# Optimization experiments

Measured on AMD Instinct MI355X. Metric: run time of the kernel, lower is better.

Reference implementation:

```python
import jax, jax.numpy as jnp
import numpy as np

B, C, O, H, W = 4, 64, 64, 96, 320


def _conv(x, w, b):
    # NCHW conv, stride 1, SAME padding (matches pad=kernel//2 in the torch code)
    out = jax.lax.conv_general_dilated(x, w, (1, 1), 'SAME',
                                       dimension_numbers=('NCHW', 'OIHW', 'NCHW'))
    return out + b[None, :, None, None]


def setup_inputs() -> dict:
    key = jax.random.key(0)
    ks = jax.random.split(key, 18)
    s = 0.05  # small init so learned offsets stay in a realistic few-pixel range
    d = {}
    d['x'] = jax.random.normal(ks[0], (B, C, H, W), jnp.float32)
    d['scale_box2d'] = jax.random.uniform(ks[1], (B, 5), jnp.float32, 0.0, 100.0)
    d['glob_w1'] = jax.random.normal(ks[2], (64, 2), jnp.float32) * s
    d['glob_b1'] = jnp.zeros((64,), jnp.float32)
    d['glob_w2'] = jax.random.normal(ks[3], (32, 64), jnp.float32) * s
    d['glob_b2'] = jnp.zeros((32,), jnp.float32)
    d['loc_w1'] = jax.random.normal(ks[4], (32, C, 3, 3), jnp.float32) * s
    d['loc_b1'] = jnp.zeros((32,), jnp.float32)
    d['loc_w2'] = jax.random.normal(ks[5], (32, 32, 1, 1), jnp.float32) * s
    d['loc_b2'] = jnp.zeros((32,), jnp.float32)
    d['fuse_w1'] = jax.random.normal(ks[6], (32, 64, 3, 3), jnp.float32) * s
    d['fuse_b1'] = jnp.zeros((32,), jnp.float32)
    d['fuse_w2'] = jax.random.normal(ks[7], (18, 32, 1, 1), jnp.float32) * s
    d['fuse_b2'] = jnp.zeros((18,), jnp.float32)
    d['mask_w'] = jnp.full((9, C, 3, 3), 0.5, jnp.float32)  # matches init_mask in torch code
    d['mask_b'] = jnp.zeros((9,), jnp.float32)
    d['conv_w'] = jax.random.normal(ks[8], (O, C, 3, 3), jnp.float32) * s
    d['conv_b'] = jax.random.normal(ks[9], (O,), jnp.float32) * s
    return d


def _deform_conv2d(x, offset, mask, weight, bias):
    # torchvision.ops.deform_conv2d, 3x3 kernel, stride 1, pad 1, dilation 1,
    # one offset group. offset channels are (dy, dx) interleaved per kernel tap.
    b, c, h, w = x.shape
    K = 9
    off = offset.reshape(b, K, 2, h, w)
    dy, dx = off[:, :, 0], off[:, :, 1]            # [B,K,H,W]
    ki = jnp.arange(3, dtype=jnp.float32) - 1.0     # kernel tap offsets with pad=1
    ky = jnp.repeat(ki, 3)                          # [9] row-major taps
    kx = jnp.tile(ki, 3)
    ys = jnp.arange(h, dtype=jnp.float32)[None, None, :, None] + ky[None, :, None, None] + dy
    xs = jnp.arange(w, dtype=jnp.float32)[None, None, None, :] + kx[None, :, None, None] + dx

    y0 = jnp.floor(ys).astype(jnp.int32)
    x0 = jnp.floor(xs).astype(jnp.int32)
    wy = (ys - y0.astype(jnp.float32))[:, None]     # [B,1,K,H,W]
    wx = (xs - x0.astype(jnp.float32))[:, None]

    xf = x.reshape(b, c, h * w)

    def gather(yi, xi):
        valid = ((yi >= 0) & (yi < h) & (xi >= 0) & (xi < w))
        yc = jnp.clip(yi, 0, h - 1)
        xc = jnp.clip(xi, 0, w - 1)
        idx = (yc * w + xc).reshape(b, 1, K * h * w)
        g = jnp.take_along_axis(xf, idx, axis=2).reshape(b, c, K, h, w)
        return g * valid.astype(x.dtype)[:, None]

    val = (gather(y0, x0) * (1 - wy) * (1 - wx)
           + gather(y0, x0 + 1) * (1 - wy) * wx
           + gather(y0 + 1, x0) * wy * (1 - wx)
           + gather(y0 + 1, x0 + 1) * wy * wx)   # [B,C,K,H,W]

    val = val * mask[:, None]                      # modulation mask [B,1,K,H,W]
    out = jnp.einsum('bckhw,ock->bohw', val, weight.reshape(weight.shape[0], c, K))
    return out + bias[None, :, None, None]


def reference(x, scale_box2d, glob_w1, glob_b1, glob_w2, glob_b2,
              loc_w1, loc_b1, loc_w2, loc_b2,
              fuse_w1, fuse_b1, fuse_w2, fuse_b2,
              mask_w, mask_b, conv_w, conv_b):
    b, c, h, w = x.shape
    bsize = jnp.stack([scale_box2d[:, 4] - scale_box2d[:, 2],
                       scale_box2d[:, 3] - scale_box2d[:, 1]], axis=-1)  # [B,2]
    g = jax.nn.relu(bsize @ glob_w1.T + glob_b1) @ glob_w2.T + glob_b2   # [B,32]
    g_offset = jnp.broadcast_to(g[:, :, None, None], (b, 32, h, w))
    l = _conv(jax.nn.relu(_conv(x, loc_w1, loc_b1)), loc_w2, loc_b2)     # [B,32,H,W]
    f = jax.nn.relu(_conv(jnp.concatenate([g_offset, l], axis=1), fuse_w1, fuse_b1))
    offset = _conv(f, fuse_w2, fuse_b2)                                  # [B,18,H,W]
    mask = jax.nn.sigmoid(_conv(x, mask_w, mask_b))                      # [B,9,H,W]
    return _deform_conv2d(x, offset, mask, conv_w, conv_b)
```

## Files before the change

kernel.cpp:

```cpp
#include <hip/hip_runtime.h>
#include <hip/hip_bf16.h>
#include <math.h>

#define BB 4
#define CC 64
#define OO 64
#define HH 96
#define WW 320
#define HWP (HH*WW)
#define NPIX (BB*HWP)

typedef __attribute__((ext_vector_type(8))) short bf16x8;
typedef __attribute__((ext_vector_type(8))) unsigned short u16x8;
typedef __attribute__((ext_vector_type(4))) float f32x4;

__device__ inline unsigned short f2bf(float f) {
    unsigned int u = __float_as_uint(f);
    u = (u + 0x7FFFu + ((u >> 16) & 1u)) >> 16;
    return (unsigned short)u;
}
__device__ inline float bf2f(unsigned short s) {
    return __uint_as_float(((unsigned int)s) << 16);
}
__device__ inline unsigned int pack2bf(float lo, float hi) {
    return (__float_as_uint(lo) >> 16) | (__float_as_uint(hi) & 0xffff0000u);
}

#define PREP_N (36864 + 27648 + 1024 + 9216 + 1024)
__global__ void k_prep(const float* __restrict__ cw,
                       const float* __restrict__ lw1, const float* __restrict__ mw,
                       const float* __restrict__ lw2,
                       const float* __restrict__ fw1, const float* __restrict__ fw2,
                       unsigned short* __restrict__ cwT,
                       unsigned short* __restrict__ Wlm,
                       unsigned short* __restrict__ lw2T,
                       unsigned short* __restrict__ Wf,
                       unsigned short* __restrict__ fw2A) {
    int e = blockIdx.x * 256 + threadIdx.x;
    if (e < 36864) {
        int k = e >> 12, r = e & 4095, o = r >> 6, ci = r & 63;
        cwT[e] = f2bf(cw[o * 576 + ci * 9 + k]);
        return;
    }
    e -= 36864;
    if (e < 27648) {
        int k = e / 3072, r = e % 3072, row = r >> 6, ci = r & 63;
        float v = 0.f;
        if (row < 32) v = lw1[row * 576 + ci * 9 + k];
        else if (row < 41) v = mw[(row - 32) * 576 + ci * 9 + k];
        Wlm[e] = f2bf(v);
        return;
    }
    e -= 27648;
    if (e < 1024) { lw2T[e] = f2bf(lw2[e]); return; }
    e -= 1024;
    if (e < 9216) {
        int k = e >> 10, r = e & 1023, o = r >> 5, cl = r & 31;
        Wf[e] = f2bf(fw1[o * 576 + (32 + cl) * 9 + k]);
        return;
    }
    e -= 9216;
    if (e < 1024) {
        int m = e >> 5, ci = e & 31;
        fw2A[e] = f2bf(m < 18 ? fw2[m * 32 + ci] : 0.f);
    }
}

__global__ void k_glob(const float* __restrict__ sb,
                       const float* __restrict__ gw1, const float* __restrict__ gb1,
                       const float* __restrict__ gw2, const float* __restrict__ gb2,
                       const float* __restrict__ fw1,
                       float* __restrict__ gsum) {
    __shared__ float g_s[BB * 32];
    int tid = threadIdx.x;
    if (tid < 128) {
        int b = tid >> 5, i = tid & 31;
        float b0 = sb[b * 5 + 4] - sb[b * 5 + 2];
        float b1 = sb[b * 5 + 3] - sb[b * 5 + 1];
        float acc = gb2[i];
        for (int j = 0; j < 64; ++j) {
            float h1 = b0 * gw1[j * 2 + 0] + b1 * gw1[j * 2 + 1] + gb1[j];
            h1 = fmaxf(h1, 0.f);
            acc += gw2[i * 64 + j] * h1;
        }
        g_s[b * 32 + i] = acc;
    }
    __syncthreads();
    for (int e = tid; e < BB * 32 * 9; e += blockDim.x) {
        int b = e / 288, r = e % 288, o = r / 9, k = r % 9;
        float s = 0.f;
        for (int ci = 0; ci < 32; ++ci)
            s += g_s[b * 32 + ci] * fw1[o * 576 + ci * 9 + k];
        gsum[e] = s;
    }
}

__global__ __launch_bounds__(256) void k_xT(const float* __restrict__ x,
                                            unsigned short* __restrict__ xT) {
    __shared__ unsigned short Ls[64 * 66];
    int tid = threadIdx.x;
    int p0 = blockIdx.x * 64;
    int b = p0 / HWP;
    int rem0 = p0 % HWP;
    int px = tid & 63;
    int g4 = tid >> 6;
    const float* xb = x + (size_t)b * CC * HWP + rem0;
#pragma unroll
    for (int it = 0; it < 16; ++it) {
        int ci = it * 4 + g4;
        Ls[px * 66 + ci] = f2bf(xb[(size_t)ci * HWP + px]);
    }
    __syncthreads();
#pragma unroll
    for (int it = 0; it < 16; ++it) {
        int p = it * 4 + g4;
        xT[(size_t)(p0 + p) * 64 + px] = Ls[p * 66 + px];
    }
}

__global__ __launch_bounds__(256) void k_locmask(
        const unsigned short* __restrict__ xT,
        const unsigned short* __restrict__ Wlm,
        const unsigned short* __restrict__ lw2T,
        const float* __restrict__ lb1, const float* __restrict__ lb2,
        const float* __restrict__ mb,
        unsigned short* __restrict__ lT, unsigned short* __restrict__ mbuf) {
    __shared__ unsigned short Vs[128 * 72];
    __shared__ unsigned short Ws[48 * 72];
    __shared__ unsigned short VsL[128 * 40];
    __shared__ unsigned short W2[32 * 40];

    int tid = threadIdx.x;
    int p0 = blockIdx.x * 128;
    int rem0 = p0 % HWP;

    int lane = tid & 63, wv = tid >> 6;
    int lr = lane & 15, lq = lane >> 4;
    int n0 = wv * 32;

    int spx = tid >> 1;
    int shf = tid & 1;
    int sy = (rem0 + spx) / WW;
    int sx = (rem0 + spx) % WW;

    f32x4 acc[3][2];
#pragma unroll
    for (int mt = 0; mt < 3; ++mt)
#pragma unroll
        for (int t = 0; t < 2; ++t) acc[mt][t] = (f32x4){0.f, 0.f, 0.f, 0.f};

    for (int k = 0; k < 9; ++k) {
        int dy = k / 3 - 1, dx = k % 3 - 1;
        __syncthreads();
#pragma unroll
        for (int c = tid; c < 384; c += 256) {
            int row = c >> 3, g = c & 7;
            *(float4*)&Ws[row * 72 + g * 8] =
                *(const float4*)&Wlm[((size_t)k * 48 + row) * 64 + g * 8];
        }
        {
            int yy = sy + dy, xw = sx + dx;
            bool valid = (yy >= 0) && (yy < HH) && (xw >= 0) && (xw < WW);
            unsigned short* dst = &Vs[spx * 72 + shf * 32];
            if (valid) {
                const unsigned short* src =
                    xT + ((size_t)(p0 + spx) + (dy * WW + dx)) * 64 + shf * 32;
#pragma unroll
                for (int j = 0; j < 4; ++j)
                    *(float4*)(dst + j * 8) = *(const float4*)(src + j * 8);
            } else {
                float4 z = {0.f, 0.f, 0.f, 0.f};
#pragma unroll
                for (int j = 0; j < 4; ++j) *(float4*)(dst + j * 8) = z;
            }
        }
        __syncthreads();
#pragma unroll
        for (int h = 0; h < 2; ++h) {
            bf16x8 b0 = *(const bf16x8*)&Vs[(n0 + lr) * 72 + h * 32 + lq * 8];
            bf16x8 b1 = *(const bf16x8*)&Vs[(n0 + 16 + lr) * 72 + h * 32 + lq * 8];
#pragma unroll
            for (int mt = 0; mt < 3; ++mt) {
                bf16x8 a = *(const bf16x8*)&Ws[(mt * 16 + lr) * 72 + h * 32 + lq * 8];
                acc[mt][0] = __builtin_amdgcn_mfma_f32_16x16x32_bf16(a, b0, acc[mt][0], 0, 0, 0);
                acc[mt][1] = __builtin_amdgcn_mfma_f32_16x16x32_bf16(a, b1, acc[mt][1], 0, 0, 0);
            }
        }
    }

#pragma unroll
    for (int c = tid; c < 128; c += 256) {
        int row = c >> 2, g = c & 3;
        *(float4*)&W2[row * 40 + g * 8] = *(const float4*)&lw2T[row * 32 + g * 8];
    }
#pragma unroll
    for (int mt = 0; mt < 2; ++mt)
#pragma unroll
        for (int t = 0; t < 2; ++t)
#pragma unroll
            for (int r = 0; r < 4; ++r) {
                int m = mt * 16 + lq * 4 + r;
                float v = acc[mt][t][r] + lb1[m];
                VsL[(n0 + t * 16 + lr) * 40 + m] = f2bf(fmaxf(v, 0.f));
            }
#pragma unroll
    for (int t = 0; t < 2; ++t)
#pragma unroll
        for (int r = 0; r < 4; ++r) {
            int j = lq * 4 + r;
            if (j < 9) {
                float v = acc[2][t][r] + mb[j];
                v = 1.f / (1.f + __expf(-v));
                mbuf[(size_t)j * NPIX + p0 + n0 + t * 16 + lr] = f2bf(v);
            }
        }
    __syncthreads();
    f32x4 acc2[2][2];
#pragma unroll
    for (int mt = 0; mt < 2; ++mt)
#pragma unroll
        for (int t = 0; t < 2; ++t) acc2[mt][t] = (f32x4){0.f, 0.f, 0.f, 0.f};
#pragma unroll
    for (int t = 0; t < 2; ++t) {
        bf16x8 b2 = *(const bf16x8*)&VsL[(n0 + t * 16 + lr) * 40 + lq * 8];
#pragma unroll
        for (int mt = 0; mt < 2; ++mt) {
            bf16x8 a2 = *(const bf16x8*)&W2[(mt * 16 + lr) * 40 + lq * 8];
            acc2[mt][t] = __builtin_amdgcn_mfma_f32_16x16x32_bf16(a2, b2, acc2[mt][t], 0, 0, 0);
        }
    }
    __syncthreads();
#pragma unroll
    for (int mt = 0; mt < 2; ++mt)
#pragma unroll
        for (int t = 0; t < 2; ++t)
#pragma unroll
            for (int r = 0; r < 4; ++r) {
                int m = mt * 16 + lq * 4 + r;
                Vs[(n0 + t * 16 + lr) * 40 + m] = f2bf(acc2[mt][t][r] + lb2[m]);
            }
    __syncthreads();
    {
        int px = tid >> 1, hf = tid & 1;
        float4 v0 = *(const float4*)&Vs[px * 40 + hf * 16];
        float4 v1 = *(const float4*)&Vs[px * 40 + hf * 16 + 8];
        unsigned short* dst = lT + (size_t)(p0 + px) * 32 + hf * 16;
        *(float4*)dst = v0;
        *(float4*)(dst + 8) = v1;
    }
}

__global__ __launch_bounds__(256) void k_fuse(
        const unsigned short* __restrict__ lT,
        const float* __restrict__ gsum,
        const unsigned short* __restrict__ Wf,
        const unsigned short* __restrict__ fw2A,
        const float* __restrict__ fb1, const float* __restrict__ fb2,
        float* __restrict__ ysA, float* __restrict__ xsA) {
    __shared__ unsigned short Vs[128 * 40];
    __shared__ unsigned short Ws[32 * 40];
    __shared__ unsigned short VsF[128 * 40];
    __shared__ unsigned short W2[32 * 40];
    __shared__ float gs[288];

    int tid = threadIdx.x;
    int p0 = blockIdx.x * 128;
    int b = p0 / HWP;
    int rem0 = p0 % HWP;

    int lane = tid & 63, wv = tid >> 6;
    int lr = lane & 15, lq = lane >> 4;
    int n0 = wv * 32;

    int spx = tid >> 1;
    int shf = tid & 1;
    int sy = (rem0 + spx) / WW;
    int sx = (rem0 + spx) % WW;

    for (int e = tid; e < 288; e += 256) gs[e] = gsum[b * 288 + e];

    f32x4 acc[2][2];
#pragma unroll
    for (int mt = 0; mt < 2; ++mt)
#pragma unroll
        for (int t = 0; t < 2; ++t) acc[mt][t] = (f32x4){0.f, 0.f, 0.f, 0.f};

    for (int k = 0; k < 9; ++k) {
        int dy = k / 3 - 1, dx = k % 3 - 1;
        __syncthreads();
#pragma unroll
        for (int c = tid; c < 128; c += 256) {
            int row = c >> 2, g = c & 3;
            *(float4*)&Ws[row * 40 + g * 8] =
                *(const float4*)&Wf[((size_t)k * 32 + row) * 32 + g * 8];
        }
        {
            int yy = sy + dy, xw = sx + dx;
            bool valid = (yy >= 0) && (yy < HH) && (xw >= 0) && (xw < WW);
            unsigned short* dst = &Vs[spx * 40 + shf * 16];
            if (valid) {
                const unsigned short* src =
                    lT + ((size_t)(p0 + spx) + (dy * WW + dx)) * 32 + shf * 16;
                *(float4*)dst = *(const float4*)src;
                *(float4*)(dst + 8) = *(const float4*)(src + 8);
            } else {
                float4 z = {0.f, 0.f, 0.f, 0.f};
                *(float4*)dst = z;
                *(float4*)(dst + 8) = z;
            }
        }
        __syncthreads();
#pragma unroll
        for (int t = 0; t < 2; ++t) {
            bf16x8 bfr = *(const bf16x8*)&Vs[(n0 + t * 16 + lr) * 40 + lq * 8];
#pragma unroll
            for (int mt = 0; mt < 2; ++mt) {
                bf16x8 a = *(const bf16x8*)&Ws[(mt * 16 + lr) * 40 + lq * 8];
                acc[mt][t] = __builtin_amdgcn_mfma_f32_16x16x32_bf16(a, bfr, acc[mt][t], 0, 0, 0);
            }
        }
    }

#pragma unroll
    for (int c = tid; c < 128; c += 256) {
        int row = c >> 2, g = c & 3;
        *(float4*)&W2[row * 40 + g * 8] = *(const float4*)&fw2A[row * 32 + g * 8];
    }
#pragma unroll
    for (int t = 0; t < 2; ++t) {
        int px = n0 + t * 16 + lr;
        int rem = rem0 + px;
        int y = rem / WW, xx = rem % WW;
        bool vk[9];
#pragma unroll
        for (int k = 0; k < 9; ++k) {
            int yy = y + k / 3 - 1, xw = xx + k % 3 - 1;
            vk[k] = (yy >= 0) && (yy < HH) && (xw >= 0) && (xw < WW);
        }
#pragma unroll
        for (int mt = 0; mt < 2; ++mt)
#pragma unroll
            for (int r = 0; r < 4; ++r) {
                int m = mt * 16 + lq * 4 + r;
                float s = fb1[m];
#pragma unroll
                for (int k = 0; k < 9; ++k)
                    if (vk[k]) s += gs[m * 9 + k];
                float v = acc[mt][t][r] + s;
                VsF[px * 40 + m] = f2bf(fmaxf(v, 0.f));
            }
    }
    __syncthreads();
    f32x4 acc3[2][2];
#pragma unroll
    for (int mt = 0; mt < 2; ++mt)
#pragma unroll
        for (int t = 0; t < 2; ++t) acc3[mt][t] = (f32x4){0.f, 0.f, 0.f, 0.f};
#pragma unroll
    for (int t = 0; t < 2; ++t) {
        bf16x8 b2 = *(const bf16x8*)&VsF[(n0 + t * 16 + lr) * 40 + lq * 8];
#pragma unroll
        for (int mt = 0; mt < 2; ++mt) {
            bf16x8 a2 = *(const bf16x8*)&W2[(mt * 16 + lr) * 40 + lq * 8];
            acc3[mt][t] = __builtin_amdgcn_mfma_f32_16x16x32_bf16(a2, b2, acc3[mt][t], 0, 0, 0);
        }
    }
#pragma unroll
    for (int t = 0; t < 2; ++t) {
        int px = n0 + t * 16 + lr;
        int p = p0 + px;
        int rem = rem0 + px;
        int y = rem / WW, xx = rem % WW;
#pragma unroll
        for (int mt = 0; mt < 2; ++mt)
#pragma unroll
            for (int r = 0; r < 4; ++r) {
                int m = mt * 16 + lq * 4 + r;
                if (m < 18) {
                    int k = m >> 1;
                    float v = acc3[mt][t][r] + fb2[m];
                    if ((m & 1) == 0)
                        ysA[(size_t)k * NPIX + p] = (float)(y + k / 3 - 1) + v;
                    else
                        xsA[(size_t)k * NPIX + p] = (float)(xx + k % 3 - 1) + v;
                }
            }
    }
}

__global__ __launch_bounds__(256) void k_deform(
        const unsigned short* __restrict__ xT,
        const unsigned short* __restrict__ cwT, const float* __restrict__ cb,
        const float* __restrict__ ysA, const float* __restrict__ xsA,
        const unsigned short* __restrict__ mA, float* __restrict__ out) {
    __shared__ unsigned short Vs[64 * 72];
    __shared__ unsigned short Ws[64 * 72];
    __shared__ float4 cfA[9 * 64];
    __shared__ int4   igA[9 * 64];

    int tid = threadIdx.x;
    int p0 = blockIdx.x * 64;
    int b = p0 / HWP;
    int rem0 = p0 % HWP;
    const unsigned short* xTb = xT + (size_t)b * HWP * 64;

    for (int e = tid; e < 9 * 64; e += 256) {
        int k = e / 64, px = e % 64;
        int p = p0 + px;
        float ys = ysA[(size_t)k * NPIX + p];
        float xs = xsA[(size_t)k * NPIX + p];
        float mk = bf2f(mA[(size_t)k * NPIX + p]);
        float y0f = floorf(ys), x0f = floorf(xs);
        int y0 = (int)y0f, x0 = (int)x0f;
        float wy = ys - y0f, wx = xs - x0f;
        float c00 = (1.f - wy) * (1.f - wx) * mk;
        float c01 = (1.f - wy) * wx * mk;
        float c10 = wy * (1.f - wx) * mk;
        float c11 = wy * wx * mk;
        bool vy0 = (y0 >= 0) && (y0 < HH);
        bool vy1 = (y0 + 1 >= 0) && (y0 + 1 < HH);
        bool vx0 = (x0 >= 0) && (x0 < WW);
        bool vx1 = (x0 + 1 >= 0) && (x0 + 1 < WW);
        c00 = (vy0 && vx0) ? c00 : 0.f;
        c01 = (vy0 && vx1) ? c01 : 0.f;
        c10 = (vy1 && vx0) ? c10 : 0.f;
        c11 = (vy1 && vx1) ? c11 : 0.f;
        int yc0 = min(max(y0, 0), HH - 1), yc1 = min(max(y0 + 1, 0), HH - 1);
        int xc0 = min(max(x0, 0), WW - 1), xc1 = min(max(x0 + 1, 0), WW - 1);
        cfA[e] = make_float4(c00, c01, c10, c11);
        igA[e] = make_int4((yc0 * WW + xc0) * 64, (yc0 * WW + xc1) * 64,
                           (yc1 * WW + xc0) * 64, (yc1 * WW + xc1) * 64);
    }

    int lane = tid & 63;
    int wv = tid >> 6;
    int m0 = wv * 16;
    int lr = lane & 15;
    int lq = lane >> 4;

    f32x4 cini;
    cini[0] = cb[m0 + lq * 4 + 0];
    cini[1] = cb[m0 + lq * 4 + 1];
    cini[2] = cb[m0 + lq * 4 + 2];
    cini[3] = cb[m0 + lq * 4 + 3];
    f32x4 acc[4];
#pragma unroll
    for (int t = 0; t < 4; ++t) acc[t] = cini;

    int sgc = tid & 15;
    int sci0 = sgc * 4;
    int spx = tid >> 4;

    for (int k = 0; k < 9; ++k) {
        __syncthreads();
#pragma unroll
        for (int c = tid; c < 512; c += 256) {
            int o = c >> 3, g = c & 7;
            *(float4*)&Ws[o * 72 + g * 8] = ((const float4*)(cwT + (size_t)k * 4096))[c];
        }
#pragma unroll
        for (int q = 0; q < 4; ++q) {
            int px = q * 16 + spx;
            float4 cc = cfA[k * 64 + px];
            int4 ii = igA[k * 64 + px];
            ushort4 u00 = *(const ushort4*)&xTb[ii.x + sci0];
            ushort4 u01 = *(const ushort4*)&xTb[ii.y + sci0];
            ushort4 u10 = *(const ushort4*)&xTb[ii.z + sci0];
            ushort4 u11 = *(const ushort4*)&xTb[ii.w + sci0];
            float v0 = cc.x * bf2f(u00.x) + cc.y * bf2f(u01.x) + cc.z * bf2f(u10.x) + cc.w * bf2f(u11.x);
            float v1 = cc.x * bf2f(u00.y) + cc.y * bf2f(u01.y) + cc.z * bf2f(u10.y) + cc.w * bf2f(u11.y);
            float v2 = cc.x * bf2f(u00.z) + cc.y * bf2f(u01.z) + cc.z * bf2f(u10.z) + cc.w * bf2f(u11.z);
            float v3 = cc.x * bf2f(u00.w) + cc.y * bf2f(u01.w) + cc.z * bf2f(u10.w) + cc.w * bf2f(u11.w);
            uint2 r;
            r.x = pack2bf(v0, v1);
            r.y = pack2bf(v2, v3);
            *(uint2*)&Vs[px * 72 + sci0] = r;
        }
        __syncthreads();
        bf16x8 a0 = *(const bf16x8*)&Ws[(m0 + lr) * 72 + lq * 8];
        bf16x8 a1 = *(const bf16x8*)&Ws[(m0 + lr) * 72 + 32 + lq * 8];
#pragma unroll
        for (int t = 0; t < 4; ++t) {
            bf16x8 b0 = *(const bf16x8*)&Vs[(t * 16 + lr) * 72 + lq * 8];
            bf16x8 b1 = *(const bf16x8*)&Vs[(t * 16 + lr) * 72 + 32 + lq * 8];
            acc[t] = __builtin_amdgcn_mfma_f32_16x16x32_bf16(a0, b0, acc[t], 0, 0, 0);
            acc[t] = __builtin_amdgcn_mfma_f32_16x16x32_bf16(a1, b1, acc[t], 0, 0, 0);
        }
    }

#pragma unroll
    for (int t = 0; t < 4; ++t) {
#pragma unroll
        for (int r = 0; r < 4; ++r) {
            int o = m0 + lq * 4 + r;
            out[(size_t)(b * 64 + o) * HWP + rem0 + t * 16 + lr] = acc[t][r];
        }
    }
}

extern "C" void kernel_launch(void* const* d_in, const int* in_sizes, int n_in,
                              void* d_out, int out_size, void* d_ws, size_t ws_size,
                              hipStream_t stream) {
    const float* x   = (const float*)d_in[0];
    const float* sb  = (const float*)d_in[1];
    const float* gw1 = (const float*)d_in[2];
    const float* gb1 = (const float*)d_in[3];
    const float* gw2 = (const float*)d_in[4];
    const float* gb2 = (const float*)d_in[5];
    const float* lw1 = (const float*)d_in[6];
    const float* lb1 = (const float*)d_in[7];
    const float* lw2 = (const float*)d_in[8];
    const float* lb2 = (const float*)d_in[9];
    const float* fw1 = (const float*)d_in[10];
    const float* fb1 = (const float*)d_in[11];
    const float* fw2 = (const float*)d_in[12];
    const float* fb2 = (const float*)d_in[13];
    const float* mw  = (const float*)d_in[14];
    const float* mb  = (const float*)d_in[15];
    const float* cw  = (const float*)d_in[16];
    const float* cb  = (const float*)d_in[17];
    float* out = (float*)d_out;

    char* w = (char*)d_ws;
    float* gsum = (float*)w;                 w += 1152 * 4;
    unsigned short* cwT  = (unsigned short*)w; w += 36864 * 2;
    unsigned short* Wlm  = (unsigned short*)w; w += 27648 * 2;
    unsigned short* lw2T = (unsigned short*)w; w += 1024 * 2;
    unsigned short* Wf   = (unsigned short*)w; w += 9216 * 2;
    unsigned short* fw2A = (unsigned short*)w; w += 1024 * 2;
    unsigned short* mbuf = (unsigned short*)w; w += (size_t)9 * NPIX * 2;
    float* ysA = (float*)w;                  w += (size_t)9 * NPIX * 4;
    float* xsA = (float*)w;                  w += (size_t)9 * NPIX * 4;
    unsigned short* xT = (unsigned short*)w; w += (size_t)NPIX * 64 * 2;
    unsigned short* lT = (unsigned short*)w;

    k_prep<<<(PREP_N + 255) / 256, 256, 0, stream>>>(cw, lw1, mw, lw2, fw1, fw2,
                                                     cwT, Wlm, lw2T, Wf, fw2A);
    k_glob<<<1, 128, 0, stream>>>(sb, gw1, gb1, gw2, gb2, fw1, gsum);
    k_xT<<<NPIX / 64, 256, 0, stream>>>(x, xT);
    k_locmask<<<NPIX / 128, 256, 0, stream>>>(xT, Wlm, lw2T, lb1, lb2, mb, lT, mbuf);
    k_fuse<<<NPIX / 128, 256, 0, stream>>>(lT, gsum, Wf, fw2A, fb1, fb2, ysA, xsA);
    k_deform<<<NPIX / 64, 256, 0, stream>>>(xT, cwT, cb, ysA, xsA, mbuf, out);
}
```

Before: 215.0 us.

## Tile loc/mask conv as 2x64 spatial patch with shared halo in LDS

The fused local/mask 3x3 conv kernel now gives each block a 2-row by 64-column pixel tile and loads a single 4x66 halo of input channels into shared memory once. Previously it reloaded shifted pixel rows from global memory for each of the 9 taps, with two barriers per tap. The weight tiles are now read straight from global memory, relying on cache, instead of being staged in LDS. This removes redundant global input traffic and most synchronisation, at the cost of a larger LDS footprint, possible bank conflicts from the shifted reads, and uncached weight loads sitting in the MFMA loop. It also assumes the grid covers 240 blocks per batch.

Result: slower. 238.1 us (+10.8%).

```diff
diff --git a/kernel.cpp b/kernel.cpp
--- a/kernel.cpp
+++ b/kernel.cpp
@@ -125,74 +125,73 @@
         const float* __restrict__ lb1, const float* __restrict__ lb2,
         const float* __restrict__ mb,
         unsigned short* __restrict__ lT, unsigned short* __restrict__ mbuf) {
-    __shared__ unsigned short Vs[128 * 72];
-    __shared__ unsigned short Ws[48 * 72];
+    __shared__ unsigned short Hs[4 * 66 * 72];
     __shared__ unsigned short VsL[128 * 40];
     __shared__ unsigned short W2[32 * 40];
 
     int tid = threadIdx.x;
-    int p0 = blockIdx.x * 128;
-    int rem0 = p0 % HWP;
+    int blk = blockIdx.x;
+    int b = blk / 240;
+    int rm = blk % 240;
+    int y0 = (rm / 5) * 2;
+    int x0 = (rm % 5) * 64;
+    int pbase = b * HWP + y0 * WW + x0;
+
+    for (int hp = tid; hp < 264; hp += 256) {
+        int r = hp / 66, c = hp % 66;
+        int gy = y0 - 1 + r, gx = x0 - 1 + c;
+        bool valid = (gy >= 0) && (gy < HH) && (gx >= 0) && (gx < WW);
+        unsigned short* dst = &Hs[hp * 72];
+        if (valid) {
+            const unsigned short* src = xT + ((size_t)b * HWP + gy * WW + gx) * 64;
+#pragma unroll
+            for (int j = 0; j < 8; ++j)
+                *(float4*)(dst + j * 8) = *(const float4*)(src + j * 8);
+        } else {
+            float4 z = {0.f, 0.f, 0.f, 0.f};
+#pragma unroll
+            for (int j = 0; j < 8; ++j) *(float4*)(dst + j * 8) = z;
+        }
+    }
+#pragma unroll
+    for (int c = tid; c < 128; c += 256) {
+        int row = c >> 2, g = c & 3;
+        *(float4*)&W2[row * 40 + g * 8] = *(const float4*)&lw2T[row * 32 + g * 8];
+    }
+    __syncthreads();
 
     int lane = tid & 63, wv = tid >> 6;
     int lr = lane & 15, lq = lane >> 4;
     int n0 = wv * 32;
 
-    int spx = tid >> 1;
-    int shf = tid & 1;
-    int sy = (rem0 + spx) / WW;
-    int sx = (rem0 + spx) % WW;
-
     f32x4 acc[3][2];
 #pragma unroll
     for (int mt = 0; mt < 3; ++mt)
 #pragma unroll
         for (int t = 0; t < 2; ++t) acc[mt][t] = (f32x4){0.f, 0.f, 0.f, 0.f};
+
+    int px0 = n0 + lr;
+    int px1 = n0 + 16 + lr;
+    int r0 = px0 >> 6, c0 = px0 & 63;
+    int r1 = px1 >> 6, c1 = px1 & 63;
 
     for (int k = 0; k < 9; ++k) {
         int dy = k / 3 - 1, dx = k % 3 - 1;
-        __syncthreads();
-#pragma unroll
-        for (int c = tid; c < 384; c += 256) {
-            int row = c >> 3, g = c & 7;
-            *(float4*)&Ws[row * 72 + g * 8] =
-                *(const float4*)&Wlm[((size_t)k * 48 + row) * 64 + g * 8];
-        }
-        {
-            int yy = sy + dy, xw = sx + dx;
-            bool valid = (yy >= 0) && (yy < HH) && (xw >= 0) && (xw < WW);
-            unsigned short* dst = &Vs[spx * 72 + shf * 32];
-            if (valid) {
-                const unsigned short* src =
-                    xT + ((size_t)(p0 + spx) + (dy * WW + dx)) * 64 + shf * 32;
-#pragma unroll
-                for (int j = 0; j < 4; ++j)
-                    *(float4*)(dst + j * 8) = *(const float4*)(src + j * 8);
-            } else {
-                float4 z = {0.f, 0.f, 0.f, 0.f};
-#pragma unroll
-                for (int j = 0; j < 4; ++j) *(float4*)(dst + j * 8) = z;
-            }
-        }
-        __syncthreads();
+        int base0 = ((r0 + dy + 1) * 66 + (c0 + dx + 1)) * 72;
+        int base1 = ((r1 + dy + 1) * 66 + (c1 + dx + 1)) * 72;
 #pragma unroll
         for (int h = 0; h < 2; ++h) {
-            bf16x8 b0 = *(const bf16x8*)&Vs[(n0 + lr) * 72 + h * 32 + lq * 8];
-            bf16x8 b1 = *(const bf16x8*)&Vs[(n0 + 16 + lr) * 72 + h * 32 + lq * 8];
+            bf16x8 b0 = *(const bf16x8*)&Hs[base0 + h * 32 + lq * 8];
+            bf16x8 b1 = *(const bf16x8*)&Hs[base1 + h * 32 + lq * 8];
 #pragma unroll
             for (int mt = 0; mt < 3; ++mt) {
-                bf16x8 a = *(const bf16x8*)&Ws[(mt * 16 + lr) * 72 + h * 32 + lq * 8];
+                bf16x8 a = *(const bf16x8*)&Wlm[((size_t)(k * 48 + mt * 16 + lr)) * 64 + h * 32 + lq * 8];
                 acc[mt][0] = __builtin_amdgcn_mfma_f32_16x16x32_bf16(a, b0, acc[mt][0], 0, 0, 0);
                 acc[mt][1] = __builtin_amdgcn_mfma_f32_16x16x32_bf16(a, b1, acc[mt][1], 0, 0, 0);
             }
         }
     }
 
-#pragma unroll
-    for (int c = tid; c < 128; c += 256) {
-        int row = c >> 2, g = c & 3;
-        *(float4*)&W2[row * 40 + g * 8] = *(const float4*)&lw2T[row * 32 + g * 8];
-    }
 #pragma unroll
     for (int mt = 0; mt < 2; ++mt)
 #pragma unroll
@@ -204,16 +203,19 @@
                 VsL[(n0 + t * 16 + lr) * 40 + m] = f2bf(fmaxf(v, 0.f));
             }
 #pragma unroll
-    for (int t = 0; t < 2; ++t)
+    for (int t = 0; t < 2; ++t) {
+        int px = n0 + t * 16 + lr;
+        int p = pbase + (px >> 6) * WW + (px & 63);
 #pragma unroll
         for (int r = 0; r < 4; ++r) {
             int j = lq * 4 + r;
             if (j < 9) {
                 float v = acc[2][t][r] + mb[j];
                 v = 1.f / (1.f + __expf(-v));
-                mbuf[(size_t)j * NPIX + p0 + n0 + t * 16 + lr] = f2bf(v);
-            }
-        }
+                mbuf[(size_t)j * NPIX + p] = f2bf(v);
+            }
+        }
+    }
     __syncthreads();
     f32x4 acc2[2][2];
 #pragma unroll
@@ -230,6 +232,7 @@
         }
     }
     __syncthreads();
+    unsigned short* SB = Hs;
 #pragma unroll
     for (int mt = 0; mt < 2; ++mt)
 #pragma unroll
@@ -237,14 +240,15 @@
 #pragma unroll
             for (int r = 0; r < 4; ++r) {
                 int m = mt * 16 + lq * 4 + r;
-                Vs[(n0 + t * 16 + lr) * 40 + m] = f2bf(acc2[mt][t][r] + lb2[m]);
+                SB[(n0 + t * 16 + lr) * 40 + m] = f2bf(acc2[mt][t][r] + lb2[m]);
             }
     __syncthreads();
     {
         int px = tid >> 1, hf = tid & 1;
-        float4 v0 = *(const float4*)&Vs[px * 40 + hf * 16];
-        float4 v1 = *(const float4*)&Vs[px * 40 + hf * 16 + 8];
-        unsigned short* dst = lT + (size_t)(p0 + px) * 32 + hf * 16;
+        int p = pbase + (px >> 6) * WW + (px & 63);
+        float4 v0 = *(const float4*)&SB[px * 40 + hf * 16];
+        float4 v1 = *(const float4*)&SB[px * 40 + hf * 16 + 8];
+        unsigned short* dst = lT + (size_t)p * 32 + hf * 16;
         *(float4*)dst = v0;
         *(float4*)(dst + 8) = v1;
     }
```
